# Kernel optimization log

Hardware: AMD Instinct MI355X
Metric: run time of the kernel (lower is better)

Reference implementation:

```python
import jax, jax.numpy as jnp
import numpy as np

B, T, F = 8192, 512, 16
H1, H2, OUT = 5, 3, 1


def _uniform(key, shape, bound):
    return jax.random.uniform(key, shape, jnp.float32, -bound, bound)


def setup_inputs() -> dict:
    key = jax.random.key(0)
    ks = jax.random.split(key, 12)
    x = jax.random.normal(ks[0], (B, T, F), dtype=jnp.float32)
    b1 = 1.0 / np.sqrt(H1)
    b2 = 1.0 / np.sqrt(H2)
    return {
        "x": x,
        "W_ih1": _uniform(ks[1], (H1, F), b1),
        "W_hh1": _uniform(ks[2], (H1, H1), b1),
        "b_ih1": _uniform(ks[3], (H1,), b1),
        "b_hh1": _uniform(ks[4], (H1,), b1),
        "W_ih2": _uniform(ks[5], (H2, H1), b2),
        "W_hh2": _uniform(ks[6], (H2, H2), b2),
        "b_ih2": _uniform(ks[7], (H2,), b2),
        "b_hh2": _uniform(ks[8], (H2,), b2),
        "W_fc": _uniform(ks[9], (OUT, H2), b2),
        "b_fc": _uniform(ks[10], (OUT,), b2),
    }


def reference(x, W_ih1, W_hh1, b_ih1, b_hh1, W_ih2, W_hh2, b_ih2, b_hh2, W_fc, b_fc):
    # Two stacked tanh-RNNs fused into one scan over time; dropout is eval-mode (identity).
    # Only the final timestep of layer 2 feeds the FC head, so no outputs are stacked.
    batch = x.shape[0]
    # Precompute input projections for layer 1 once: [B,T,H1] -> scan over T.
    xproj = jnp.einsum('btf,hf->tbh', x, W_ih1) + (b_ih1 + b_hh1)

    def step(carry, xp_t):
        h1, h2 = carry
        h1 = jnp.tanh(xp_t + h1 @ W_hh1.T)
        h2 = jnp.tanh(h1 @ W_ih2.T + h2 @ W_hh2.T + (b_ih2 + b_hh2))
        return (h1, h2), None

    h1_0 = jnp.zeros((batch, W_hh1.shape[0]), dtype=x.dtype)
    h2_0 = jnp.zeros((batch, W_hh2.shape[0]), dtype=x.dtype)
    (h1, h2), _ = jax.lax.scan(step, (h1_0, h2_0), xproj)
    return jax.nn.sigmoid(h2 @ W_fc.T + b_fc)  # [B, 1]
```

## Files before the change

kernel.cpp:

```cpp
#include <hip/hip_runtime.h>


namespace {

constexpr int kB  = 8192;
constexpr int kT  = 512;
constexpr int kF  = 16;
constexpr int kH1 = 5;
constexpr int kH2 = 3;

constexpr int SPB = 32;
constexpr int C   = 16;
constexpr int NC  = kT / C;

__device__ __forceinline__ float fast_tanh(float v) {
    float e = __expf(v + v);
    return 1.0f - __fdividef(2.0f, e + 1.0f);
}

__device__ __forceinline__ void load_chunk(const float4* __restrict__ xs,
                                           int k, int plane, float4 nb[4][4]) {
#pragma unroll
    for (int i = 0; i < 4; ++i) {
        const int tg = k * C + plane + 4 * i;
#pragma unroll
        for (int q = 0; q < 4; ++q) nb[i][q] = xs[tg * 4 + q];
    }
}

__global__ __launch_bounds__(256) void rnn_pipe_kernel(
    const float* __restrict__ x,
    const float* __restrict__ W_ih1,
    const float* __restrict__ W_hh1,
    const float* __restrict__ b_ih1,
    const float* __restrict__ b_hh1,
    const float* __restrict__ W_ih2,
    const float* __restrict__ W_hh2,
    const float* __restrict__ b_ih2,
    const float* __restrict__ b_hh2,
    const float* __restrict__ W_fc,
    const float* __restrict__ b_fc,
    float* __restrict__ out)
{
    __shared__ float xp [2][C][kH1][SPB];
    __shared__ float h1r[2][C][kH1][SPB];

    const int tid  = threadIdx.x;
    const int wave = tid >> 6;
    const int lane = tid & 63;
    const int s    = lane & 31;
    const bool act = (lane < 32);

    if (wave >= 2) {
        const int plane = (wave - 2) * 2 + (lane >> 5);
        float w1[kH1][kF], bs1[kH1];
#pragma unroll
        for (int h = 0; h < kH1; ++h) {
            bs1[h] = b_ih1[h] + b_hh1[h];
#pragma unroll
            for (int f = 0; f < kF; ++f) w1[h][f] = W_ih1[h * kF + f];
        }
        const float4* xs = reinterpret_cast<const float4*>(x) +
                           (size_t)(blockIdx.x * SPB + s) * (kT * 4);

        float4 nb[4][4];
        load_chunk(xs, 0, plane, nb);

        for (int k = 0; k < NC + 2; ++k) {
            if (k < NC) {
                const int buf = k & 1;
#pragma unroll
                for (int i = 0; i < 4; ++i) {
                    const int tl = plane + 4 * i;
                    const float xv[kF] = {
                        nb[i][0].x, nb[i][0].y, nb[i][0].z, nb[i][0].w,
                        nb[i][1].x, nb[i][1].y, nb[i][1].z, nb[i][1].w,
                        nb[i][2].x, nb[i][2].y, nb[i][2].z, nb[i][2].w,
                        nb[i][3].x, nb[i][3].y, nb[i][3].z, nb[i][3].w};
#pragma unroll
                    for (int h = 0; h < kH1; ++h) {
                        float acc = bs1[h];
#pragma unroll
                        for (int f = 0; f < kF; ++f)
                            acc = fmaf(xv[f], w1[h][f], acc);
                        xp[buf][tl][h][s] = acc;
                    }
                }
                if (k + 1 < NC) load_chunk(xs, k + 1, plane, nb);
            }
            __syncthreads();
        }
    } else if (wave == 0) {
        float whh1[kH1][kH1];
#pragma unroll
        for (int h = 0; h < kH1; ++h)
#pragma unroll
            for (int j = 0; j < kH1; ++j) whh1[h][j] = W_hh1[h * kH1 + j];

        float h1[kH1] = {0.f, 0.f, 0.f, 0.f, 0.f};

        for (int k = 0; k < NC + 2; ++k) {
            if (k >= 1 && k <= NC && act) {
                const int buf = (k - 1) & 1;
#pragma unroll 4
                for (int t = 0; t < C; ++t) {
                    float a[kH1];
#pragma unroll
                    for (int h = 0; h < kH1; ++h) {
                        float acc = xp[buf][t][h][s];
#pragma unroll
                        for (int j = 0; j < kH1; ++j)
                            acc = fmaf(h1[j], whh1[h][j], acc);
                        a[h] = acc;
                    }
#pragma unroll
                    for (int h = 0; h < kH1; ++h) {
                        h1[h] = fast_tanh(a[h]);
                        h1r[buf][t][h][s] = h1[h];
                    }
                }
            }
            __syncthreads();
        }
    } else {
        float wih2[kH2][kH1], whh2[kH2][kH2], bs2[kH2], wfc[kH2];
#pragma unroll
        for (int m = 0; m < kH2; ++m) {
            bs2[m] = b_ih2[m] + b_hh2[m];
            wfc[m] = W_fc[m];
#pragma unroll
            for (int j = 0; j < kH1; ++j) wih2[m][j] = W_ih2[m * kH1 + j];
#pragma unroll
            for (int j = 0; j < kH2; ++j) whh2[m][j] = W_hh2[m * kH2 + j];
        }
        const float bfc = b_fc[0];

        float h2[kH2] = {0.f, 0.f, 0.f};

        for (int k = 0; k < NC + 2; ++k) {
            if (k >= 2 && act) {
                const int buf = (k - 2) & 1;
#pragma unroll 4
                for (int t = 0; t < C; ++t) {
                    float h1v[kH1];
#pragma unroll
                    for (int j = 0; j < kH1; ++j) h1v[j] = h1r[buf][t][j][s];
                    float c[kH2];
#pragma unroll
                    for (int m = 0; m < kH2; ++m) {
                        float acc = bs2[m];
#pragma unroll
                        for (int j = 0; j < kH1; ++j)
                            acc = fmaf(h1v[j], wih2[m][j], acc);
#pragma unroll
                        for (int j = 0; j < kH2; ++j)
                            acc = fmaf(h2[j], whh2[m][j], acc);
                        c[m] = acc;
                    }
#pragma unroll
                    for (int m = 0; m < kH2; ++m) h2[m] = fast_tanh(c[m]);
                }
            }
            __syncthreads();
        }

        if (act) {
            float z = bfc;
#pragma unroll
            for (int m = 0; m < kH2; ++m) z = fmaf(h2[m], wfc[m], z);
            out[blockIdx.x * SPB + s] =
                __fdividef(1.0f, 1.0f + __expf(-z));
        }
    }
}

}

extern "C" void kernel_launch(void* const* d_in, const int* in_sizes, int n_in,
                              void* d_out, int out_size, void* d_ws, size_t ws_size,
                              hipStream_t stream) {
    const float* x     = (const float*)d_in[0];
    const float* W_ih1 = (const float*)d_in[1];
    const float* W_hh1 = (const float*)d_in[2];
    const float* b_ih1 = (const float*)d_in[3];
    const float* b_hh1 = (const float*)d_in[4];
    const float* W_ih2 = (const float*)d_in[5];
    const float* W_hh2 = (const float*)d_in[6];
    const float* b_ih2 = (const float*)d_in[7];
    const float* b_hh2 = (const float*)d_in[8];
    const float* W_fc  = (const float*)d_in[9];
    const float* b_fc  = (const float*)d_in[10];
    float* out = (float*)d_out;

    dim3 grid(kB / SPB), block(256);
    rnn_pipe_kernel<<<grid, block, 0, stream>>>(
        x, W_ih1, W_hh1, b_ih1, b_hh1, W_ih2, W_hh2, b_ih2, b_hh2, W_fc, b_fc,
        out);
}
```

Baseline: 418.1 us.

## Split fused RNN into separate projection kernel and per-thread register scan

Replaces the single warp-specialized kernel, which passed data between waves through shared memory with a block barrier at every chunk, with two kernels. The first computes the layer-1 input projection for all timesteps into a workspace buffer in time-major layout. The second runs both recurrences per batch element in registers, one thread per element, double-buffering chunks of 8 timesteps loaded from global memory. This removes the per-chunk barriers and the handoff between waves, but it adds a round trip of about 84MB through global memory and leaves the scan with only 128 blocks of 64 threads, which is very low occupancy on a large GPU.

```diff
diff --git a/kernel.cpp b/kernel.cpp
--- a/kernel.cpp
+++ b/kernel.cpp
@@ -2,38 +2,72 @@
 
 
 namespace {
-
 constexpr int kB  = 8192;
 constexpr int kT  = 512;
 constexpr int kF  = 16;
 constexpr int kH1 = 5;
 constexpr int kH2 = 3;
 
-constexpr int SPB = 32;
-constexpr int C   = 16;
-constexpr int NC  = kT / C;
+constexpr int TC = 32;
+constexpr int CH = 8;
+
+typedef float v4 __attribute__((ext_vector_type(4), aligned(4)));
 
 __device__ __forceinline__ float fast_tanh(float v) {
     float e = __expf(v + v);
     return 1.0f - __fdividef(2.0f, e + 1.0f);
 }
+}
 
-__device__ __forceinline__ void load_chunk(const float4* __restrict__ xs,
-                                           int k, int plane, float4 nb[4][4]) {
+__global__ __launch_bounds__(256) void rnn_p1_xproj(
+    const float* __restrict__ x,
+    const float* __restrict__ W_ih1,
+    const float* __restrict__ b_ih1,
+    const float* __restrict__ b_hh1,
+    float* __restrict__ xp)
+{
+    const int gid = blockIdx.x * 256 + threadIdx.x;
+    const int b   = gid & (kB - 1);
+    const int tc  = gid >> 13;
+
+    float w1[kH1][kF], bs[kH1];
 #pragma unroll
-    for (int i = 0; i < 4; ++i) {
-        const int tg = k * C + plane + 4 * i;
+    for (int h = 0; h < kH1; ++h) {
+        bs[h] = b_ih1[h] + b_hh1[h];
 #pragma unroll
-        for (int q = 0; q < 4; ++q) nb[i][q] = xs[tg * 4 + q];
+        for (int f = 0; f < kF; ++f) w1[h][f] = W_ih1[h * kF + f];
+    }
+
+    const float4* xb = reinterpret_cast<const float4*>(x) +
+                       ((size_t)b * kT + (size_t)tc * TC) * 4;
+
+#pragma unroll 4
+    for (int j = 0; j < TC; ++j) {
+        const float4 q0 = xb[j * 4 + 0];
+        const float4 q1 = xb[j * 4 + 1];
+        const float4 q2 = xb[j * 4 + 2];
+        const float4 q3 = xb[j * 4 + 3];
+        const float xv[kF] = {q0.x, q0.y, q0.z, q0.w, q1.x, q1.y, q1.z, q1.w,
+                              q2.x, q2.y, q2.z, q2.w, q3.x, q3.y, q3.z, q3.w};
+        float a[kH1];
+#pragma unroll
+        for (int h = 0; h < kH1; ++h) {
+            float acc = bs[h];
+#pragma unroll
+            for (int f = 0; f < kF; ++f) acc = fmaf(xv[f], w1[h][f], acc);
+            a[h] = acc;
+        }
+        const int t = tc * TC + j;
+        float* p = xp + ((size_t)t * kB + b) * 5;
+        v4 q; q[0] = a[0]; q[1] = a[1]; q[2] = a[2]; q[3] = a[3];
+        *reinterpret_cast<v4*>(p) = q;
+        p[4] = a[4];
     }
 }
 
-__global__ __launch_bounds__(256) void rnn_pipe_kernel(
-    const float* __restrict__ x,
-    const float* __restrict__ W_ih1,
+__global__ __launch_bounds__(64) void rnn_p2_scan(
+    const float* __restrict__ xp,
     const float* __restrict__ W_hh1,
-    const float* __restrict__ b_ih1,
-    const float* __restrict__ b_hh1,
     const float* __restrict__ W_ih2,
     const float* __restrict__ W_hh2,
     const float* __restrict__ b_ih2,
@@ -42,138 +76,90 @@
     const float* __restrict__ b_fc,
     float* __restrict__ out)
 {
-    __shared__ float xp [2][C][kH1][SPB];
-    __shared__ float h1r[2][C][kH1][SPB];
+    const int b = blockIdx.x * 64 + threadIdx.x;
 
-    const int tid  = threadIdx.x;
-    const int wave = tid >> 6;
-    const int lane = tid & 63;
-    const int s    = lane & 31;
-    const bool act = (lane < 32);
+    float whh1[kH1][kH1];
+#pragma unroll
+    for (int h = 0; h < kH1; ++h)
+#pragma unroll
+        for (int j = 0; j < kH1; ++j) whh1[h][j] = W_hh1[h * kH1 + j];
 
-    if (wave >= 2) {
-        const int plane = (wave - 2) * 2 + (lane >> 5);
-        float w1[kH1][kF], bs1[kH1];
+    float wih2[kH2][kH1], whh2[kH2][kH2], bs2[kH2], wfc[kH2];
 #pragma unroll
-        for (int h = 0; h < kH1; ++h) {
-            bs1[h] = b_ih1[h] + b_hh1[h];
+    for (int m = 0; m < kH2; ++m) {
+        bs2[m] = b_ih2[m] + b_hh2[m];
+        wfc[m] = W_fc[m];
 #pragma unroll
-            for (int f = 0; f < kF; ++f) w1[h][f] = W_ih1[h * kF + f];
+        for (int j = 0; j < kH1; ++j) wih2[m][j] = W_ih2[m * kH1 + j];
+#pragma unroll
+        for (int j = 0; j < kH2; ++j) whh2[m][j] = W_hh2[m * kH2 + j];
+    }
+    const float bfc = b_fc[0];
+
+    float h1[kH1] = {0.f, 0.f, 0.f, 0.f, 0.f};
+    float h2[kH2] = {0.f, 0.f, 0.f};
+
+    const char* basep = reinterpret_cast<const char*>(xp + (size_t)b * 5);
+    constexpr size_t TSTRIDE = (size_t)kB * 5 * sizeof(float);
+
+    v4 A4[CH]; float A1[CH];
+    v4 B4[CH]; float B1[CH];
+
+    auto LOADC = [&](v4* Q4, float* Q1, int c) {
+#pragma unroll
+        for (int i = 0; i < CH; ++i) {
+            const float* p = reinterpret_cast<const float*>(
+                basep + (size_t)(c * CH + i) * TSTRIDE);
+            Q4[i] = *reinterpret_cast<const v4*>(p);
+            Q1[i] = p[4];
         }
-        const float4* xs = reinterpret_cast<const float4*>(x) +
-                           (size_t)(blockIdx.x * SPB + s) * (kT * 4);
+    };
 
-        float4 nb[4][4];
-        load_chunk(xs, 0, plane, nb);
+    auto STEP8 = [&](const v4* Q4, const float* Q1) {
+#pragma unroll
+        for (int i = 0; i < CH; ++i) {
+            float a[kH1];
+#pragma unroll
+            for (int h = 0; h < kH1; ++h) {
+                float acc = (h < 4) ? Q4[i][h] : Q1[i];
+#pragma unroll
+                for (int j = 0; j < kH1; ++j)
+                    acc = fmaf(h1[j], whh1[h][j], acc);
+                a[h] = acc;
+            }
+#pragma unroll
+            for (int h = 0; h < kH1; ++h) h1[h] = fast_tanh(a[h]);
 
-        for (int k = 0; k < NC + 2; ++k) {
-            if (k < NC) {
-                const int buf = k & 1;
+            float c2[kH2];
 #pragma unroll
-                for (int i = 0; i < 4; ++i) {
-                    const int tl = plane + 4 * i;
-                    const float xv[kF] = {
-                        nb[i][0].x, nb[i][0].y, nb[i][0].z, nb[i][0].w,
-                        nb[i][1].x, nb[i][1].y, nb[i][1].z, nb[i][1].w,
-                        nb[i][2].x, nb[i][2].y, nb[i][2].z, nb[i][2].w,
-                        nb[i][3].x, nb[i][3].y, nb[i][3].z, nb[i][3].w};
+            for (int m = 0; m < kH2; ++m) {
+                float acc = bs2[m];
 #pragma unroll
-                    for (int h = 0; h < kH1; ++h) {
-                        float acc = bs1[h];
+                for (int j = 0; j < kH1; ++j)
+                    acc = fmaf(h1[j], wih2[m][j], acc);
 #pragma unroll
-                        for (int f = 0; f < kF; ++f)
-                            acc = fmaf(xv[f], w1[h][f], acc);
-                        xp[buf][tl][h][s] = acc;
-                    }
-                }
-                if (k + 1 < NC) load_chunk(xs, k + 1, plane, nb);
+                for (int j = 0; j < kH2; ++j)
+                    acc = fmaf(h2[j], whh2[m][j], acc);
+                c2[m] = acc;
             }
-            __syncthreads();
+#pragma unroll
+            for (int m = 0; m < kH2; ++m) h2[m] = fast_tanh(c2[m]);
         }
-    } else if (wave == 0) {
-        float whh1[kH1][kH1];
+    };
+
+    LOADC(A4, A1, 0);
+    constexpr int NCH = kT / CH;
+    for (int c = 0; c < NCH; c += 2) {
+        LOADC(B4, B1, c + 1);
+        STEP8(A4, A1);
+        if (c + 2 < NCH) LOADC(A4, A1, c + 2);
+        STEP8(B4, B1);
+    }
+
+    float z = bfc;
 #pragma unroll
-        for (int h = 0; h < kH1; ++h)
-#pragma unroll
-            for (int j = 0; j < kH1; ++j) whh1[h][j] = W_hh1[h * kH1 + j];
-
-        float h1[kH1] = {0.f, 0.f, 0.f, 0.f, 0.f};
-
-        for (int k = 0; k < NC + 2; ++k) {
-            if (k >= 1 && k <= NC && act) {
-                const int buf = (k - 1) & 1;
-#pragma unroll 4
-                for (int t = 0; t < C; ++t) {
-                    float a[kH1];
-#pragma unroll
-                    for (int h = 0; h < kH1; ++h) {
-                        float acc = xp[buf][t][h][s];
-#pragma unroll
-                        for (int j = 0; j < kH1; ++j)
-                            acc = fmaf(h1[j], whh1[h][j], acc);
-                        a[h] = acc;
-                    }
-#pragma unroll
-                    for (int h = 0; h < kH1; ++h) {
-                        h1[h] = fast_tanh(a[h]);
-                        h1r[buf][t][h][s] = h1[h];
-                    }
-                }
-            }
-            __syncthreads();
-        }
-    } else {
-        float wih2[kH2][kH1], whh2[kH2][kH2], bs2[kH2], wfc[kH2];
-#pragma unroll
-        for (int m = 0; m < kH2; ++m) {
-            bs2[m] = b_ih2[m] + b_hh2[m];
-            wfc[m] = W_fc[m];
-#pragma unroll
-            for (int j = 0; j < kH1; ++j) wih2[m][j] = W_ih2[m * kH1 + j];
-#pragma unroll
-            for (int j = 0; j < kH2; ++j) whh2[m][j] = W_hh2[m * kH2 + j];
-        }
-        const float bfc = b_fc[0];
-
-        float h2[kH2] = {0.f, 0.f, 0.f};
-
-        for (int k = 0; k < NC + 2; ++k) {
-            if (k >= 2 && act) {
-                const int buf = (k - 2) & 1;
-#pragma unroll 4
-                for (int t = 0; t < C; ++t) {
-                    float h1v[kH1];
-#pragma unroll
-                    for (int j = 0; j < kH1; ++j) h1v[j] = h1r[buf][t][j][s];
-                    float c[kH2];
-#pragma unroll
-                    for (int m = 0; m < kH2; ++m) {
-                        float acc = bs2[m];
-#pragma unroll
-                        for (int j = 0; j < kH1; ++j)
-                            acc = fmaf(h1v[j], wih2[m][j], acc);
-#pragma unroll
-                        for (int j = 0; j < kH2; ++j)
-                            acc = fmaf(h2[j], whh2[m][j], acc);
-                        c[m] = acc;
-                    }
-#pragma unroll
-                    for (int m = 0; m < kH2; ++m) h2[m] = fast_tanh(c[m]);
-                }
-            }
-            __syncthreads();
-        }
-
-        if (act) {
-            float z = bfc;
-#pragma unroll
-            for (int m = 0; m < kH2; ++m) z = fmaf(h2[m], wfc[m], z);
-            out[blockIdx.x * SPB + s] =
-                __fdividef(1.0f, 1.0f + __expf(-z));
-        }
-    }
-}
-
+    for (int m = 0; m < kH2; ++m) z = fmaf(h2[m], wfc[m], z);
+    out[b] = __fdividef(1.0f, 1.0f + __expf(-z));
 }
 
 extern "C" void kernel_launch(void* const* d_in, const int* in_sizes, int n_in,
@@ -191,9 +177,9 @@
     const float* W_fc  = (const float*)d_in[9];
     const float* b_fc  = (const float*)d_in[10];
     float* out = (float*)d_out;
+    float* xp  = (float*)d_ws;
 
-    dim3 grid(kB / SPB), block(256);
-    rnn_pipe_kernel<<<grid, block, 0, stream>>>(
-        x, W_ih1, W_hh1, b_ih1, b_hh1, W_ih2, W_hh2, b_ih2, b_hh2, W_fc, b_fc,
-        out);
+    rnn_p1_xproj<<<dim3(512), dim3(256), 0, stream>>>(x, W_ih1, b_ih1, b_hh1, xp);
+    rnn_p2_scan<<<dim3(128), dim3(64), 0, stream>>>(
+        xp, W_hh1, W_ih2, W_hh2, b_ih2, b_hh2, W_fc, b_fc, out);
 }
```

Measured after the change: 588.8 us. 40.8% more time.
